# Kernel tuning notes

Hardware: AMD Instinct MI355X
Metric: run time of the kernel (lower is better)

## Reference

```python
import jax, jax.numpy as jnp
import numpy as np

ALPHA = 0.2  # leaky_relu negative slope


def setup_inputs() -> dict:
    key = jax.random.key(0)
    k1, k2, k3, k4 = jax.random.split(key, 4)
    B, N, Din, Dout = 8, 2048, 64, 64
    x = jax.random.normal(k1, (B, N, Din), dtype=jnp.float32)
    adj = (jax.random.uniform(k2, (N, N)) < 0.05).astype(jnp.float32)
    # xavier_uniform init for weight and a
    lim_w = float(np.sqrt(6.0 / (Din + Dout)))
    weight = jax.random.uniform(k3, (Din, Dout), dtype=jnp.float32, minval=-lim_w, maxval=lim_w)
    lim_a = float(np.sqrt(6.0 / (2 * Dout + 1)))
    a = jax.random.uniform(k4, (2 * Dout, 1), dtype=jnp.float32, minval=-lim_a, maxval=lim_a)
    bias = jnp.zeros((Dout,), dtype=jnp.float32)
    return {"x": x, "adj": adj, "weight": weight, "a": a, "bias": bias}


def reference(x, adj, weight, a, bias):
    # eval mode: dropout is identity
    N = adj.shape[0]
    adj = adj.at[jnp.diag_indices(N)].set(1.0)  # fill_diagonal_(1)
    h = jnp.einsum('bni,io->bno', x, weight)    # [B,N,D]
    D = h.shape[-1]
    # e_ij = leaky_relu(h_i . a[:D] + h_j . a[D:])  (equiv to concat+matmul with a)
    e_src = h @ a[:D, 0]                        # [B,N]
    e_dst = h @ a[D:, 0]                        # [B,N]
    e = jax.nn.leaky_relu(e_src[:, :, None] + e_dst[:, None, :], negative_slope=ALPHA)
    e = adj[None, :, :] * e                     # multiplicative mask (as in source)
    attention = jax.nn.softmax(e, axis=-1)      # [B,N,N]
    h_prime = jnp.einsum('bij,bjd->bid', attention, h)
    return h_prime + bias
```

## Files before the change

kernel.cpp:

```cpp
#include <hip/hip_runtime.h>
#include <hip/hip_bf16.h>


constexpr int Bq = 8;
constexpr int Nq = 2048;
constexpr int MAXL = 256;
#define ALPHA 0.2f

__global__ __launch_bounds__(256) void proj_kernel(
    const float* __restrict__ x, const float* __restrict__ W,
    const float* __restrict__ a, __hip_bfloat16* __restrict__ h_bf,
    float* __restrict__ s_t, float* __restrict__ dv_t,
    float* __restrict__ hsumv) {
  __shared__ float red[4][64];
  const int tid = threadIdx.x;
  const int lane = tid & 63;
  const int wv = tid >> 6;

  float Wc[64];
#pragma unroll
  for (int k = 0; k < 64; ++k) Wc[k] = W[k * 64 + lane];

  const int row0 = __builtin_amdgcn_readfirstlane((int)blockIdx.x * 16 + wv * 4);
  const float* __restrict__ xr = x + (size_t)row0 * 64;

  float acc[4] = {0.f, 0.f, 0.f, 0.f};
#pragma unroll
  for (int k = 0; k < 64; ++k) {
    const float w = Wc[k];
    acc[0] = fmaf(xr[k], w, acc[0]);
    acc[1] = fmaf(xr[64 + k], w, acc[1]);
    acc[2] = fmaf(xr[128 + k], w, acc[2]);
    acc[3] = fmaf(xr[192 + k], w, acc[3]);
  }

  const float aS = a[lane], aD = a[64 + lane];
#pragma unroll
  for (int r = 0; r < 4; ++r) {
    const int row = row0 + r;
    const int b = row >> 11, n = row & 2047;
    h_bf[(size_t)n * 512 + b * 64 + lane] = __float2bfloat16(acc[r]);
    float ps = acc[r] * aS, pd = acc[r] * aD;
#pragma unroll
    for (int off = 32; off; off >>= 1) {
      ps += __shfl_xor(ps, off);
      pd += __shfl_xor(pd, off);
    }
    if (lane == 0) {
      s_t[n * 8 + b] = ps;
      dv_t[n * 8 + b] = pd;
    }
  }
  red[wv][lane] = acc[0] + acc[1] + acc[2] + acc[3];
  __syncthreads();
  if (wv == 0) {
    const int b = blockIdx.x >> 7;
    atomicAdd(&hsumv[b * 64 + lane],
              red[0][lane] + red[1][lane] + red[2][lane] + red[3][lane]);
  }
}

__global__ __launch_bounds__(256) void attn_kernel(
    const float* __restrict__ adj, const __hip_bfloat16* __restrict__ h_bf,
    const float* __restrict__ s_t, const float* __restrict__ dv_t,
    const float* __restrict__ hsumv, const float* __restrict__ bias,
    float* __restrict__ out) {
  __shared__ int sJ[MAXL];
  __shared__ float sacc[4][512];
  __shared__ float szz[4][8];
  __shared__ int scnt;
  const int i = blockIdx.x;
  const int tid = threadIdx.x;
  const int lane = tid & 63;
  const int wv = tid >> 6;

  if (tid == 0) scnt = 0;
  __syncthreads();

  float av[8];
#pragma unroll
  for (int c = 0; c < 8; ++c)
    av[c] = __builtin_nontemporal_load(
        &adj[(size_t)i * Nq + wv * 64 + c * 256 + lane]);
#pragma unroll
  for (int c = 0; c < 8; ++c) {
    const int j = wv * 64 + c * 256 + lane;
    const bool nz = (av[c] != 0.0f) || (j == i);
    unsigned long long m = __ballot(nz);
    const int cnt = __popcll(m);
    int base = 0;
    if (lane == 0 && cnt) base = atomicAdd(&scnt, cnt);
    base = __shfl(base, 0);
    if (nz) sJ[base + __popcll(m & ((1ULL << lane) - 1))] = j;
  }
  __syncthreads();
  const int L = scnt;

  const int g2 = lane >> 3;
  const int lbase = lane * 8;
  const float sg = s_t[i * 8 + g2];
  float acc[8] = {0.f, 0.f, 0.f, 0.f, 0.f, 0.f, 0.f, 0.f};
  float Zp = 0.f;

#define GAT_ACC(hc, dc)                                          \
  {                                                              \
    float t = sg + (dc);                                         \
    t = (t >= 0.f) ? t : ALPHA * t;                              \
    const float w = __expf(t) - 1.0f;                            \
    Zp += w;                                                     \
    const unsigned u0 = (hc).x, u1 = (hc).y;                     \
    const unsigned u2 = (hc).z, u3 = (hc).w;                     \
    acc[0] = fmaf(w, __uint_as_float(u0 << 16), acc[0]);         \
    acc[1] = fmaf(w, __uint_as_float(u0 & 0xffff0000u), acc[1]); \
    acc[2] = fmaf(w, __uint_as_float(u1 << 16), acc[2]);         \
    acc[3] = fmaf(w, __uint_as_float(u1 & 0xffff0000u), acc[3]); \
    acc[4] = fmaf(w, __uint_as_float(u2 << 16), acc[4]);         \
    acc[5] = fmaf(w, __uint_as_float(u2 & 0xffff0000u), acc[5]); \
    acc[6] = fmaf(w, __uint_as_float(u3 << 16), acc[6]);         \
    acc[7] = fmaf(w, __uint_as_float(u3 & 0xffff0000u), acc[7]); \
  }

  int e = wv;
  uint4 hA, hB;
  float dA = 0.f, dB = 0.f;
  bool hvA = e < L;
  bool hvB = (e + 4) < L;
  if (hvA) {
    const int j = sJ[e];
    dA = dv_t[j * 8 + g2];
    hA = *(const uint4*)(h_bf + (size_t)j * 512 + lbase);
  }
  if (hvB) {
    const int j = sJ[e + 4];
    dB = dv_t[j * 8 + g2];
    hB = *(const uint4*)(h_bf + (size_t)j * 512 + lbase);
  }
  while (hvA) {
    const uint4 hcA = hA;
    const float dcA = dA;
    const bool hvA2 = (e + 8) < L;
    if (hvA2) {
      const int j = sJ[e + 8];
      dA = dv_t[j * 8 + g2];
      hA = *(const uint4*)(h_bf + (size_t)j * 512 + lbase);
    }
    GAT_ACC(hcA, dcA);
    if (!hvB) break;
    const uint4 hcB = hB;
    const float dcB = dB;
    const bool hvB2 = (e + 12) < L;
    if (hvB2) {
      const int j = sJ[e + 12];
      dB = dv_t[j * 8 + g2];
      hB = *(const uint4*)(h_bf + (size_t)j * 512 + lbase);
    }
    GAT_ACC(hcB, dcB);
    e += 8;
    hvA = hvA2;
    hvB = hvB2;
  }
#undef GAT_ACC

  if ((lane & 7) == 0) szz[wv][g2] = Zp;

  *(float4*)&sacc[wv][lbase] = make_float4(acc[0], acc[1], acc[2], acc[3]);
  *(float4*)&sacc[wv][lbase + 4] = make_float4(acc[4], acc[5], acc[6], acc[7]);
  __syncthreads();

#pragma unroll
  for (int half = 0; half < 2; ++half) {
    const int ei = tid + half * 256;
    const float v = sacc[0][ei] + sacc[1][ei] + sacc[2][ei] + sacc[3][ei];
    const int b = ei >> 6, d = ei & 63;
    const float Z = (float)Nq + szz[0][b] + szz[1][b] + szz[2][b] + szz[3][b];
    out[(size_t)(b * Nq + i) * 64 + d] =
        (hsumv[ei] + v) * __builtin_amdgcn_rcpf(Z) + bias[d];
  }
}

extern "C" void kernel_launch(void* const* d_in, const int* in_sizes, int n_in,
                              void* d_out, int out_size, void* d_ws,
                              size_t ws_size, hipStream_t stream) {
  const float* x = (const float*)d_in[0];
  const float* adj = (const float*)d_in[1];
  const float* W = (const float*)d_in[2];
  const float* a = (const float*)d_in[3];
  const float* bias = (const float*)d_in[4];
  float* out = (float*)d_out;

  float* s_t = (float*)d_ws;
  float* dv_t = s_t + (size_t)Nq * Bq;
  float* hsumv = dv_t + (size_t)Nq * Bq;
  __hip_bfloat16* h_bf = (__hip_bfloat16*)(hsumv + 512);

  hipMemsetAsync(hsumv, 0, 512 * sizeof(float), stream);
  proj_kernel<<<1024, 256, 0, stream>>>(x, W, a, h_bf, s_t, dv_t, hsumv);
  attn_kernel<<<Nq, 256, 0, stream>>>(adj, h_bf, s_t, dv_t, hsumv, bias, out);
}
```

Measured before the change: 105.6 us.

## Move adjacency compaction into projection kernel and pass neighbor lists via workspace

Each projection block now also reads two adjacency rows and compacts their nonzero column indices into a global per-row list (up to MAXL entries) with a count. The attention kernel only loads this precomputed list instead of scanning the 16 MB adjacency row itself. The aim is to overlap the adjacency stream with the projection math and shorten the attention kernel's critical path. It adds global writes and reads of the index lists, and the MAXL=256 cap is assumed safe for about 5% density.

```diff
diff --git a/kernel.cpp b/kernel.cpp
--- a/kernel.cpp
+++ b/kernel.cpp
@@ -9,19 +9,32 @@
 
 __global__ __launch_bounds__(256) void proj_kernel(
     const float* __restrict__ x, const float* __restrict__ W,
-    const float* __restrict__ a, __hip_bfloat16* __restrict__ h_bf,
-    float* __restrict__ s_t, float* __restrict__ dv_t,
-    float* __restrict__ hsumv) {
+    const float* __restrict__ a, const float* __restrict__ adj,
+    __hip_bfloat16* __restrict__ h_bf, float* __restrict__ s_t,
+    float* __restrict__ dv_t, float* __restrict__ hsumv,
+    int* __restrict__ sJG, int* __restrict__ cntG) {
   __shared__ float red[4][64];
+  __shared__ int scnt[2];
   const int tid = threadIdx.x;
   const int lane = tid & 63;
   const int wv = tid >> 6;
+  if (tid < 2) scnt[tid] = 0;
+
+  const int n0 = (int)blockIdx.x * 2;
+  float av[2][8];
+#pragma unroll
+  for (int r = 0; r < 2; ++r)
+#pragma unroll
+    for (int c = 0; c < 8; ++c)
+      av[r][c] = __builtin_nontemporal_load(
+          &adj[(size_t)(n0 + r) * Nq + c * 256 + tid]);
 
   float Wc[64];
 #pragma unroll
   for (int k = 0; k < 64; ++k) Wc[k] = W[k * 64 + lane];
 
-  const int row0 = __builtin_amdgcn_readfirstlane((int)blockIdx.x * 16 + wv * 4);
+  const int row0 =
+      __builtin_amdgcn_readfirstlane((int)blockIdx.x * 16 + wv * 4);
   const float* __restrict__ xr = x + (size_t)row0 * 64;
 
   float acc[4] = {0.f, 0.f, 0.f, 0.f};
@@ -53,48 +66,49 @@
   }
   red[wv][lane] = acc[0] + acc[1] + acc[2] + acc[3];
   __syncthreads();
+
+#pragma unroll
+  for (int r = 0; r < 2; ++r) {
+    const int n = n0 + r;
+#pragma unroll
+    for (int c = 0; c < 8; ++c) {
+      const int j = c * 256 + tid;
+      const bool nz = (av[r][c] != 0.0f) || (j == n);
+      unsigned long long m = __ballot(nz);
+      const int cnt = __popcll(m);
+      int base = 0;
+      if (lane == 0 && cnt) base = atomicAdd(&scnt[r], cnt);
+      base = __shfl(base, 0);
+      if (nz)
+        sJG[(size_t)n * MAXL + base + __popcll(m & ((1ULL << lane) - 1))] = j;
+    }
+  }
+
   if (wv == 0) {
-    const int b = blockIdx.x >> 7;
+    const int b = (int)blockIdx.x >> 7;
     atomicAdd(&hsumv[b * 64 + lane],
               red[0][lane] + red[1][lane] + red[2][lane] + red[3][lane]);
   }
+  __syncthreads();
+  if (tid < 2) cntG[n0 + tid] = scnt[tid];
 }
 
 __global__ __launch_bounds__(256) void attn_kernel(
-    const float* __restrict__ adj, const __hip_bfloat16* __restrict__ h_bf,
-    const float* __restrict__ s_t, const float* __restrict__ dv_t,
-    const float* __restrict__ hsumv, const float* __restrict__ bias,
-    float* __restrict__ out) {
+    const int* __restrict__ cntG, const int* __restrict__ sJG,
+    const __hip_bfloat16* __restrict__ h_bf, const float* __restrict__ s_t,
+    const float* __restrict__ dv_t, const float* __restrict__ hsumv,
+    const float* __restrict__ bias, float* __restrict__ out) {
   __shared__ int sJ[MAXL];
   __shared__ float sacc[4][512];
   __shared__ float szz[4][8];
-  __shared__ int scnt;
   const int i = blockIdx.x;
   const int tid = threadIdx.x;
   const int lane = tid & 63;
   const int wv = tid >> 6;
 
-  if (tid == 0) scnt = 0;
-  __syncthreads();
-
-  float av[8];
-#pragma unroll
-  for (int c = 0; c < 8; ++c)
-    av[c] = __builtin_nontemporal_load(
-        &adj[(size_t)i * Nq + wv * 64 + c * 256 + lane]);
-#pragma unroll
-  for (int c = 0; c < 8; ++c) {
-    const int j = wv * 64 + c * 256 + lane;
-    const bool nz = (av[c] != 0.0f) || (j == i);
-    unsigned long long m = __ballot(nz);
-    const int cnt = __popcll(m);
-    int base = 0;
-    if (lane == 0 && cnt) base = atomicAdd(&scnt, cnt);
-    base = __shfl(base, 0);
-    if (nz) sJ[base + __popcll(m & ((1ULL << lane) - 1))] = j;
-  }
-  __syncthreads();
-  const int L = scnt;
+  sJ[tid] = sJG[(size_t)i * MAXL + tid];
+  const int L = cntG[i];
+  __syncthreads();
 
   const int g2 = lane >> 3;
   const int lbase = lane * 8;
@@ -192,8 +206,12 @@
   float* dv_t = s_t + (size_t)Nq * Bq;
   float* hsumv = dv_t + (size_t)Nq * Bq;
   __hip_bfloat16* h_bf = (__hip_bfloat16*)(hsumv + 512);
+  int* cntG = (int*)(h_bf + (size_t)Nq * 512);
+  int* sJG = cntG + Nq;
 
   hipMemsetAsync(hsumv, 0, 512 * sizeof(float), stream);
-  proj_kernel<<<1024, 256, 0, stream>>>(x, W, a, h_bf, s_t, dv_t, hsumv);
-  attn_kernel<<<Nq, 256, 0, stream>>>(adj, h_bf, s_t, dv_t, hsumv, bias, out);
+  proj_kernel<<<1024, 256, 0, stream>>>(x, W, a, adj, h_bf, s_t, dv_t, hsumv,
+                                        sJG, cntG);
+  attn_kernel<<<Nq, 256, 0, stream>>>(cntG, sJG, h_bf, s_t, dv_t, hsumv, bias,
+                                      out);
 }
```

Result: no change. 106.9 us (+1.2%).
